# Kernel optimization log

Hardware: AMD Instinct MI355X
Metric: run time of the kernel (lower is better)

Reference implementation:

```python
import jax, jax.numpy as jnp
import numpy as np

MARGIN = 0.7
ITERS = 1000  # as hard-coded in ot_loss's log_optimal_transport call


def setup_inputs() -> dict:
    key = jax.random.key(0)
    k1, k2 = jax.random.split(key)
    # features: N x C x W x H  (query at index 0, 8 targets)
    x = jax.random.normal(k1, (9, 256, 32, 32), dtype=jnp.float32)
    # attention: N x W x H, strictly positive since it is logged directly
    att = jax.random.uniform(k2, (9, 32, 32), dtype=jnp.float32, minval=0.1, maxval=1.0)
    return {"x": x, "att": att, "label": 1}


def _ot_distance(x, att):
    N, C, W, H = x.shape
    m = W * H              # number of query locations
    n = (N - 1) * W * H    # number of target locations
    Q = x[0].reshape(C, m).T                                          # (m, C)
    T = x[1:].reshape(N - 1, C, m).transpose(0, 2, 1).reshape(n, C)   # (n, C)
    mu = att[0].reshape(m)      # query marginal
    nu = att[1:].reshape(n)     # target marginal
    # pairwise squared euclidean distances (m, n)
    M = (jnp.sum(Q * Q, axis=1)[:, None]
         + jnp.sum(T * T, axis=1)[None, :]
         - 2.0 * (Q @ T.T))
    log_mu = jnp.log(mu)
    log_nu = jnp.log(nu)

    def step(carry, _):
        u, v = carry
        u = log_mu - jax.nn.logsumexp(M + v[None, :], axis=1)
        v = log_nu - jax.nn.logsumexp(M + u[:, None], axis=0)
        return (u, v), None

    init = (jnp.zeros((m,), M.dtype), jnp.zeros((n,), M.dtype))
    (u, v), _ = jax.lax.scan(jax.checkpoint(step), init, None, length=ITERS)
    P = jnp.exp(M + u[:, None] + v[None, :])   # transport plan (m, n)
    # OT barycentric distance per query location, summed
    diff = mu[:, None] * Q - P @ T             # (m, C)
    return jnp.sqrt(jnp.sum(diff * diff, axis=1)).sum()


def reference(x, att, label):
    d = _ot_distance(x, att)
    if label:  # label is a concrete python int: positive pair
        return d
    return jnp.clip(MARGIN - d, 0.0, None)
```

## Files before the change

### kernel.cpp

```cpp
#include <hip/hip_runtime.h>
#include <math.h>

#define MR 1024
#define NC 8192
#define NCH 256
#define OT_ITERS 1000
#define IMG_STRIDE 262144
#define PBLK 512

__device__ inline float wredMax(float v){
#pragma unroll
  for (int m = 32; m >= 1; m >>= 1) v = fmaxf(v, __shfl_xor(v, m, 64));
  return v;
}
__device__ inline float wredMin(float v){
#pragma unroll
  for (int m = 32; m >= 1; m >>= 1) v = fminf(v, __shfl_xor(v, m, 64));
  return v;
}
__device__ inline float wredSum(float v){
#pragma unroll
  for (int m = 32; m >= 1; m >>= 1) v += __shfl_xor(v, m, 64);
  return v;
}

__device__ inline unsigned fkey(float f){
  unsigned b = __float_as_uint(f);
  return (b & 0x80000000u) ? ~b : (b | 0x80000000u);
}
__device__ inline float funkey(unsigned k){
  return (k & 0x80000000u) ? __uint_as_float(k & 0x7fffffffu) : __uint_as_float(~k);
}

__global__ __launch_bounds__(256) void kPrep(const float* __restrict__ x,
                                             const float* __restrict__ att,
                                             float* __restrict__ qq, float* __restrict__ tt,
                                             float* __restrict__ logmu, float* __restrict__ lognu,
                                             float* __restrict__ u, float* __restrict__ v,
                                             float* __restrict__ acc, unsigned* __restrict__ prmI,
                                             int* __restrict__ bar){
  int idx = blockIdx.x * 256 + threadIdx.x;
  if (idx < 9216){
    int img = idx >> 10, pos = idx & 1023;
    const float* p = x + img * IMG_STRIDE + pos;
    float s = 0.f;
#pragma unroll 8
    for (int c = 0; c < NCH; ++c){ float a = p[c * 1024]; s += a * a; }
    float lg = logf(att[idx]);
    if (img == 0){ qq[idx] = s;        logmu[idx] = lg; }
    else         { tt[idx - 1024] = s; lognu[idx - 1024] = lg; }
  }
  if (idx < MR) u[idx] = 0.f;
  if (idx < NC) v[idx] = 0.f;
  if (idx < 1024) bar[idx] = 0;
  if (idx == 0){ *acc = 0.f; prmI[0] = 0xFFFFFFFFu; prmI[1] = 0u; }
}

__global__ __launch_bounds__(256) void kGemmM(const float* __restrict__ x,
                                              const float* __restrict__ qq,
                                              const float* __restrict__ tt,
                                              float* __restrict__ M,
                                              unsigned* __restrict__ prmI){
  __shared__ float As[16][68];
  __shared__ float Bs[16][68];
  __shared__ float smn[4], smx[4];
  int jb = blockIdx.x;
  int ib = blockIdx.y;
  int i0 = ib * 64;
  int j0 = jb * 64;
  int k  = j0 >> 10, p0 = j0 & 1023;
  const float* A = x + i0;
  const float* B = x + (1 + k) * IMG_STRIDE + p0;
  int tid = threadIdx.x;
  int lr = tid >> 4, lc = (tid & 15) * 4;
  int ty = tid >> 4, tx = tid & 15;
  float accv[4][4] = {};
  for (int kt = 0; kt < 16; ++kt){
    int c = kt * 16 + lr;
    float4 av = *(const float4*)(A + c * 1024 + lc);
    float4 bv = *(const float4*)(B + c * 1024 + lc);
    *(float4*)(&As[lr][lc]) = av;
    *(float4*)(&Bs[lr][lc]) = bv;
    __syncthreads();
#pragma unroll
    for (int kk = 0; kk < 16; ++kk){
      float4 a = *(const float4*)(&As[kk][ty * 4]);
      float4 b = *(const float4*)(&Bs[kk][tx * 4]);
// ... 35 lines not shown
__global__ __launch_bounds__(256) void kQuantTrans(const float* __restrict__ M,
                                                   unsigned short* __restrict__ Mq,
                                                   unsigned short* __restrict__ Mtq,
                                                   float* __restrict__ prm){
  __shared__ float tile[64][65];
  const unsigned* prmI = (const unsigned*)prm;
  float mn = funkey(prmI[0]);
  float mx = funkey(prmI[1]);
  float rng = mx - mn;
  float inv = (rng > 0.f) ? 65535.0f / rng : 0.f;
  float sc  = (rng > 0.f) ? rng / 65535.0f : 0.f;
  int i0 = blockIdx.y * 64;
  int j0 = blockIdx.x * 64;
  int t = threadIdx.x;
  int tc = t & 63, tr = t >> 6;
#pragma unroll
  for (int rr = 0; rr < 64; rr += 4)
    tile[rr + tr][tc] = M[(long)(i0 + rr + tr) * NC + j0 + tc];
  __syncthreads();
#pragma unroll
  for (int rr = 0; rr < 64; rr += 4){
    float a = tile[rr + tr][tc];
    int qa = (int)lrintf((a - mn) * inv);
    qa = qa < 0 ? 0 : (qa > 65535 ? 65535 : qa);
    Mq[(long)(i0 + rr + tr) * NC + j0 + tc] = (unsigned short)qa;
    float b = tile[tc][rr + tr];
    int qb = (int)lrintf((b - mn) * inv);
    qb = qb < 0 ? 0 : (qb > 65535 ? 65535 : qb);
    Mtq[(long)(j0 + rr + tr) * MR + i0 + tc] = (unsigned short)qb;
  }
  if (blockIdx.x == 0 && blockIdx.y == 0 && t == 0){ prm[2] = mn; prm[3] = sc; }
}

__device__ inline void gbar(int* bar, int g, int ep){
  __syncthreads();
  if (threadIdx.x == 0){
    asm volatile("s_waitcnt vmcnt(0)" ::: "memory");
    int a = __hip_atomic_fetch_add(&bar[g * 32], 1, __ATOMIC_RELAXED, __HIP_MEMORY_SCOPE_AGENT);
    if (a == 64 * ep - 1){
      int go = __hip_atomic_fetch_add(&bar[512], 1, __ATOMIC_RELAXED, __HIP_MEMORY_SCOPE_AGENT);
      if (go == 8 * ep - 1){
#pragma unroll
        for (int g2 = 0; g2 < 8; ++g2)
          __hip_atomic_store(&bar[256 + g2 * 32], ep, __ATOMIC_RELAXED, __HIP_MEMORY_SCOPE_AGENT);
      }
    }
    while (__hip_atomic_load(&bar[256 + g * 32], __ATOMIC_RELAXED, __HIP_MEMORY_SCOPE_AGENT) < ep)
      __builtin_amdgcn_s_sleep(4);
  }
  __syncthreads();
}

__global__ __launch_bounds__(256, 2) void kSink2(const unsigned short* __restrict__ Mq,
                                                 const unsigned short* __restrict__ Mtq,
                                                 const float* __restrict__ logmu,
                                                 const float* __restrict__ lognu,
                                                 float* __restrict__ u,
                                                 float* __restrict__ v,
                                                 const float* __restrict__ prm,
                                                 int* __restrict__ bar){
  __shared__ float sh[8192];
  __shared__ float redA0[4], redA1[4], redB0[4], redB1[4];
  int tid = threadIdx.x, b = blockIdx.x;
  int lane = tid & 63, w = tid >> 6;
  int g = b & 7;
  float mn = prm[2], s = prm[3];
  int r0 = 2 * b;
  const unsigned short* R0 = Mq + (long)r0 * NC;
  const unsigned short* R1 = R0 + NC;
  float lmu0 = logmu[r0], lmu1 = logmu[r0 + 1];
  float lnu[4];
#pragma unroll
  for (int cc = 0; cc < 4; ++cc) lnu[cc] = lognu[16 * b + w * 4 + cc];
  int ep = 0;

  for (int it = 0; it < OT_ITERS; ++it){
#pragma unroll
    for (int h = 0; h < 2; ++h){
      float tmp[16];
#pragma unroll
      for (int q = 0; q < 16; ++q)
        tmp[q] = __hip_atomic_load(v + (h * 16 + q) * 256 + tid, __ATOMIC_RELAXED, __HIP_MEMORY_SCOPE_AGENT);
#pragma unroll
      for (int q = 0; q < 16; ++q)
        sh[(h * 16 + q) * 256 + tid] = tmp[q];
    }
    __syncthreads();
    float t0[32], t1[32];
    float mx0 = -INFINITY, mx1 = -INFINITY;
#pragma unroll
    for (int kb = 0; kb < 4; ++kb){
      int cidx = kb * 2048 + tid * 8;
      uint4 qa = *(const uint4*)(R0 + cidx);
      uint4 qb = *(const uint4*)(R1 + cidx);
      float4 v0 = *(const float4*)(&sh[cidx]);
      float4 v1 = *(const float4*)(&sh[cidx + 4]);
      float a0 = fmaf(s, (float)(qa.x & 0xFFFFu), v0.x);
      float a1 = fmaf(s, (float)(qa.x >> 16),     v0.y);
      float a2 = fmaf(s, (float)(qa.y & 0xFFFFu), v0.z);
      float a3 = fmaf(s, (float)(qa.y >> 16),     v0.w);
      float a4 = fmaf(s, (float)(qa.z & 0xFFFFu), v1.x);
      float a5 = fmaf(s, (float)(qa.z >> 16),     v1.y);
      float a6 = fmaf(s, (float)(qa.w & 0xFFFFu), v1.z);
      float a7 = fmaf(s, (float)(qa.w >> 16),     v1.w);
      float c0 = fmaf(s, (float)(qb.x & 0xFFFFu), v0.x);
      float c1 = fmaf(s, (float)(qb.x >> 16),     v0.y);
      float c2 = fmaf(s, (float)(qb.y & 0xFFFFu), v0.z);
      float c3 = fmaf(s, (float)(qb.y >> 16),     v0.w);
      float c4 = fmaf(s, (float)(qb.z & 0xFFFFu), v1.x);
      float c5 = fmaf(s, (float)(qb.z >> 16),     v1.y);
      float c6 = fmaf(s, (float)(qb.w & 0xFFFFu), v1.z);
      float c7 = fmaf(s, (float)(qb.w >> 16),     v1.w);
      t0[kb*8+0]=a0; t0[kb*8+1]=a1; t0[kb*8+2]=a2; t0[kb*8+3]=a3;
      t0[kb*8+4]=a4; t0[kb*8+5]=a5; t0[kb*8+6]=a6; t0[kb*8+7]=a7;
      t1[kb*8+0]=c0; t1[kb*8+1]=c1; t1[kb*8+2]=c2; t1[kb*8+3]=c3;
      t1[kb*8+4]=c4; t1[kb*8+5]=c5; t1[kb*8+6]=c6; t1[kb*8+7]=c7;
      mx0 = fmaxf(mx0, fmaxf(fmaxf(fmaxf(a0,a1),fmaxf(a2,a3)), fmaxf(fmaxf(a4,a5),fmaxf(a6,a7))));
      mx1 = fmaxf(mx1, fmaxf(fmaxf(fmaxf(c0,c1),fmaxf(c2,c3)), fmaxf(fmaxf(c4,c5),fmaxf(c6,c7))));
    }
    float wm0 = wredMax(mx0), wm1 = wredMax(mx1);
    if (lane == 0){ redA0[w] = wm0; redA1[w] = wm1; }
    __syncthreads();
    float bm0 = fmaxf(fmaxf(redA0[0], redA0[1]), fmaxf(redA0[2], redA0[3]));
    float bm1 = fmaxf(fmaxf(redA1[0], redA1[1]), fmaxf(redA1[2], redA1[3]));
    float s0 = 0.f, s1 = 0.f;
#pragma unroll
    for (int q = 0; q < 32; ++q){ s0 += __expf(t0[q] - bm0); s1 += __expf(t1[q] - bm1); }
    s0 = wredSum(s0); s1 = wredSum(s1);
    if (lane == 0){ redB0[w] = s0; redB1[w] = s1; }
    __syncthreads();
    if (tid == 0){
      float nu0 = lmu0 - mn - (bm0 + __logf(redB0[0] + redB0[1] + redB0[2] + redB0[3]));
      float nu1 = lmu1 - mn - (bm1 + __logf(redB1[0] + redB1[1] + redB1[2] + redB1[3]));
      __hip_atomic_store(u + r0,     nu0, __ATOMIC_RELAXED, __HIP_MEMORY_SCOPE_AGENT);
      __hip_atomic_store(u + r0 + 1, nu1, __ATOMIC_RELAXED, __HIP_MEMORY_SCOPE_AGENT);
    }
    gbar(bar, g, ++ep);

    {
      float tu[4];
#pragma unroll
      for (int q = 0; q < 4; ++q)
        tu[q] = __hip_atomic_load(u + q * 256 + tid, __ATOMIC_RELAXED, __HIP_MEMORY_SCOPE_AGENT);
#pragma unroll
      for (int q = 0; q < 4; ++q) sh[q * 256 + tid] = tu[q];
    }
    __syncthreads();
#pragma unroll
    for (int cc = 0; cc < 4; ++cc){
      int j = 16 * b + w * 4 + cc;
      const unsigned short* R = Mtq + (long)j * MR;
      uint4 qa = *(const uint4*)(R + lane * 8);
      uint4 qb = *(const uint4*)(R + 512 + lane * 8);
      float4 ua0 = *(const float4*)(&sh[lane * 8]);
      float4 ua1 = *(const float4*)(&sh[lane * 8 + 4]);
      float4 ub0 = *(const float4*)(&sh[512 + lane * 8]);
      float4 ub1 = *(const float4*)(&sh[512 + lane * 8 + 4]);
      float tv[16];
      tv[0]  = fmaf(s, (float)(qa.x & 0xFFFFu), ua0.x);
      tv[1]  = fmaf(s, (float)(qa.x >> 16),     ua0.y);
      tv[2]  = fmaf(s, (float)(qa.y & 0xFFFFu), ua0.z);
      tv[3]  = fmaf(s, (float)(qa.y >> 16),     ua0.w);
      tv[4]  = fmaf(s, (float)(qa.z & 0xFFFFu), ua1.x);
      tv[5]  = fmaf(s, (float)(qa.z >> 16),     ua1.y);
      tv[6]  = fmaf(s, (float)(qa.w & 0xFFFFu), ua1.z);
      tv[7]  = fmaf(s, (float)(qa.w >> 16),     ua1.w);
      tv[8]  = fmaf(s, (float)(qb.x & 0xFFFFu), ub0.x);
      tv[9]  = fmaf(s, (float)(qb.x >> 16),     ub0.y);
      tv[10] = fmaf(s, (float)(qb.y & 0xFFFFu), ub0.z);
      tv[11] = fmaf(s, (float)(qb.y >> 16),     ub0.w);
      tv[12] = fmaf(s, (float)(qb.z & 0xFFFFu), ub1.x);
      tv[13] = fmaf(s, (float)(qb.z >> 16),     ub1.y);
      tv[14] = fmaf(s, (float)(qb.w & 0xFFFFu), ub1.z);
      tv[15] = fmaf(s, (float)(qb.w >> 16),     ub1.w);
      float mx = -INFINITY;
#pragma unroll
      for (int q = 0; q < 16; ++q) mx = fmaxf(mx, tv[q]);
      mx = wredMax(mx);
      float sm = 0.f;
#pragma unroll
      for (int q = 0; q < 16; ++q) sm += __expf(tv[q] - mx);
      sm = wredSum(sm);
      if (lane == 0)
        __hip_atomic_store(v + j, lnu[cc] - mn - (mx + __logf(sm)),
                           __ATOMIC_RELAXED, __HIP_MEMORY_SCOPE_AGENT);
    }
    gbar(bar, g, ++ep);
  }
}

__global__ __launch_bounds__(256) void kUPassQ(const unsigned short* __restrict__ Mq,
                                               const float* __restrict__ v,
                                               const float* __restrict__ logmu,
                                               float* __restrict__ u,
                                               const float* __restrict__ prm){
  int b = blockIdx.x, tid = threadIdx.x;
  float mn = prm[2], s = prm[3];
  int r0 = 2 * b;
  const unsigned short* R0 = Mq + (long)r0 * NC;
  const unsigned short* R1 = R0 + NC;
  float t0[32], t1[32];
  float mx0 = -INFINITY, mx1 = -INFINITY;
#pragma unroll
  for (int kb = 0; kb < 4; ++kb){
    int cidx = kb * 2048 + tid * 8;
    uint4 qa = *(const uint4*)(R0 + cidx);
    uint4 qb = *(const uint4*)(R1 + cidx);
    float4 v0 = *(const float4*)(v + cidx);
    float4 v1 = *(const float4*)(v + cidx + 4);
    float a0 = fmaf(s, (float)(qa.x & 0xFFFFu), v0.x);
    float a1 = fmaf(s, (float)(qa.x >> 16),     v0.y);
    float a2 = fmaf(s, (float)(qa.y & 0xFFFFu), v0.z);
    float a3 = fmaf(s, (float)(qa.y >> 16),     v0.w);
    float a4 = fmaf(s, (float)(qa.z & 0xFFFFu), v1.x);
    float a5 = fmaf(s, (float)(qa.z >> 16),     v1.y);
    float a6 = fmaf(s, (float)(qa.w & 0xFFFFu), v1.z);
    float a7 = fmaf(s, (float)(qa.w >> 16),     v1.w);
    float c0 = fmaf(s, (float)(qb.x & 0xFFFFu), v0.x);
    float c1 = fmaf(s, (float)(qb.x >> 16),     v0.y);
    float c2 = fmaf(s, (float)(qb.y & 0xFFFFu), v0.z);
    float c3 = fmaf(s, (float)(qb.y >> 16),     v0.w);
    float c4 = fmaf(s, (float)(qb.z & 0xFFFFu), v1.x);
    float c5 = fmaf(s, (float)(qb.z >> 16),     v1.y);
    float c6 = fmaf(s, (float)(qb.w & 0xFFFFu), v1.z);
    float c7 = fmaf(s, (float)(qb.w >> 16),     v1.w);
    t0[kb*8+0]=a0; t0[kb*8+1]=a1; t0[kb*8+2]=a2; t0[kb*8+3]=a3;
    t0[kb*8+4]=a4; t0[kb*8+5]=a5; t0[kb*8+6]=a6; t0[kb*8+7]=a7;
    t1[kb*8+0]=c0; t1[kb*8+1]=c1; t1[kb*8+2]=c2; t1[kb*8+3]=c3;
    t1[kb*8+4]=c4; t1[kb*8+5]=c5; t1[kb*8+6]=c6; t1[kb*8+7]=c7;
    mx0 = fmaxf(mx0, fmaxf(fmaxf(fmaxf(a0,a1),fmaxf(a2,a3)), fmaxf(fmaxf(a4,a5),fmaxf(a6,a7))));
    mx1 = fmaxf(mx1, fmaxf(fmaxf(fmaxf(c0,c1),fmaxf(c2,c3)), fmaxf(fmaxf(c4,c5),fmaxf(c6,c7))));
  }
  __shared__ float redA0[4], redA1[4], redB0[4], redB1[4];
  int lane = tid & 63, w = tid >> 6;
  float wm0 = wredMax(mx0), wm1 = wredMax(mx1);
  if (lane == 0){ redA0[w] = wm0; redA1[w] = wm1; }
  __syncthreads();
  float bm0 = fmaxf(fmaxf(redA0[0], redA0[1]), fmaxf(redA0[2], redA0[3]));
  float bm1 = fmaxf(fmaxf(redA1[0], redA1[1]), fmaxf(redA1[2], redA1[3]));
  float s0 = 0.f, s1 = 0.f;
#pragma unroll
  for (int q = 0; q < 32; ++q){ s0 += __expf(t0[q] - bm0); s1 += __expf(t1[q] - bm1); }
  s0 = wredSum(s0); s1 = wredSum(s1);
  if (lane == 0){ redB0[w] = s0; redB1[w] = s1; }
  __syncthreads();
  if (tid == 0){
    u[r0]     = logmu[r0]     - mn - (bm0 + __logf(redB0[0] + redB0[1] + redB0[2] + redB0[3]));
    u[r0 + 1] = logmu[r0 + 1] - mn - (bm1 + __logf(redB1[0] + redB1[1] + redB1[2] + redB1[3]));
  }
}

__global__ __launch_bounds__(256) void kVPassQ(const unsigned short* __restrict__ Mtq,
                                               const float* __restrict__ u,
                                               const float* __restrict__ lognu,
                                               float* __restrict__ v,
                                               const float* __restrict__ prm){
  __shared__ float ulds[1024];
  int tid = threadIdx.x;
  float mn = prm[2], s = prm[3];
  *(float4*)(&ulds[tid * 4]) = *(const float4*)(u + tid * 4);
  __syncthreads();
  int w = tid >> 6, lane = tid & 63;
#pragma unroll
  for (int cc = 0; cc < 4; ++cc){
    int j = blockIdx.x * 16 + w * 4 + cc;
    const unsigned short* R = Mtq + (long)j * MR;
    uint4 qa = *(const uint4*)(R + lane * 8);
    uint4 qb = *(const uint4*)(R + 512 + lane * 8);
    float4 ua0 = *(const float4*)(&ulds[lane * 8]);
    float4 ua1 = *(const float4*)(&ulds[lane * 8 + 4]);
    float4 ub0 = *(const float4*)(&ulds[512 + lane * 8]);
    float4 ub1 = *(const float4*)(&ulds[512 + lane * 8 + 4]);
    float tv[16];
    tv[0]  = fmaf(s, (float)(qa.x & 0xFFFFu), ua0.x);
    tv[1]  = fmaf(s, (float)(qa.x >> 16),     ua0.y);
    tv[2]  = fmaf(s, (float)(qa.y & 0xFFFFu), ua0.z);
    tv[3]  = fmaf(s, (float)(qa.y >> 16),     ua0.w);
    tv[4]  = fmaf(s, (float)(qa.z & 0xFFFFu), ua1.x);
    tv[5]  = fmaf(s, (float)(qa.z >> 16),     ua1.y);
    tv[6]  = fmaf(s, (float)(qa.w & 0xFFFFu), ua1.z);
    tv[7]  = fmaf(s, (float)(qa.w >> 16),     ua1.w);
    tv[8]  = fmaf(s, (float)(qb.x & 0xFFFFu), ub0.x);
    tv[9]  = fmaf(s, (float)(qb.x >> 16),     ub0.y);
    tv[10] = fmaf(s, (float)(qb.y & 0xFFFFu), ub0.z);
    tv[11] = fmaf(s, (float)(qb.y >> 16),     ub0.w);
    tv[12] = fmaf(s, (float)(qb.z & 0xFFFFu), ub1.x);
    tv[13] = fmaf(s, (float)(qb.z >> 16),     ub1.y);
    tv[14] = fmaf(s, (float)(qb.w & 0xFFFFu), ub1.z);
    tv[15] = fmaf(s, (float)(qb.w >> 16),     ub1.w);
    float mx = -INFINITY;
#pragma unroll
    for (int q = 0; q < 16; ++q) mx = fmaxf(mx, tv[q]);
    mx = wredMax(mx);
    float sm = 0.f;
#pragma unroll
    for (int q = 0; q < 16; ++q) sm += __expf(tv[q] - mx);
    sm = wredSum(sm);
    if (lane == 0) v[j] = lognu[j] - mn - (mx + __logf(sm));
  }
}

__global__ __launch_bounds__(256) void kFinal(const float* __restrict__ x,
                                              const float* __restrict__ att,
                                              const float* __restrict__ M,
                                              const float* __restrict__ u,
                                              const float* __restrict__ v,
                                              float* __restrict__ acc){
  __shared__ float pch[4][256];
  __shared__ float redS[4];
  int tid = threadIdx.x;
  int r0 = blockIdx.x * 4;
  float u4[4];
#pragma unroll
  for (int rr = 0; rr < 4; ++rr) u4[rr] = u[r0 + rr];
  float o[4] = {0.f, 0.f, 0.f, 0.f};
  for (int jc = 0; jc < NC; jc += 256){
    float vv = v[jc + tid];
#pragma unroll
    for (int rr = 0; rr < 4; ++rr)
      pch[rr][tid] = __expf(M[(long)(r0 + rr) * NC + jc + tid] + u4[rr] + vv);
    __syncthreads();
    int k = jc >> 10;
    const float* Tp = x + (1 + k) * IMG_STRIDE + tid * 1024 + (jc & 1023);
    for (int jj = 0; jj < 256; jj += 4){
      float4 tv = *(const float4*)(Tp + jj);
      float tq[4] = {tv.x, tv.y, tv.z, tv.w};
#pragma unroll
      for (int q = 0; q < 4; ++q){
        o[0] += pch[0][jj + q] * tq[q];
        o[1] += pch[1][jj + q] * tq[q];
        o[2] += pch[2][jj + q] * tq[q];
        o[3] += pch[3][jj + q] * tq[q];
      }
    }
    __syncthreads();
  }
  int lane = tid & 63, wid = tid >> 6;
  float dtot = 0.f;
#pragma unroll
  for (int rr = 0; rr < 4; ++rr){
    float mu = att[r0 + rr];
    float qv = x[tid * 1024 + (r0 + rr)];
    float diff = mu * qv - o[rr];
    float wsum = wredSum(diff * diff);
    if (lane == 0) redS[wid] = wsum;
    __syncthreads();
    if (tid == 0) dtot += sqrtf(redS[0] + redS[1] + redS[2] + redS[3]);
    __syncthreads();
  }
  if (tid == 0) atomicAdd(acc, dtot);
}

__global__ void kOut(const float* __restrict__ acc, const int* __restrict__ label,
                     float* __restrict__ out){
  if (threadIdx.x == 0 && blockIdx.x == 0){
    float d = *acc;
    out[0] = (*label) ? d : fmaxf(0.7f - d, 0.f);
  }
}

extern "C" void kernel_launch(void* const* d_in, const int* in_sizes, int n_in,
                              void* d_out, int out_size, void* d_ws, size_t ws_size,
                              hipStream_t stream){
  const float* x   = (const float*)d_in[0];
  const float* att = (const float*)d_in[1];
  const int* label = (const int*)d_in[2];
  float* W = (float*)d_ws;
  float* out = (float*)d_out;

  float* M = W;
  unsigned short* Mq  = (unsigned short*)(W + 8388608);
  unsigned short* Mtq = (unsigned short*)(W + 8388608 + 4194304);
  float* S     = W + 16777216;
  float* qq    = S;
  float* tt    = qq + 1024;
  float* logmu = tt + 8192;
  float* lognu = logmu + 1024;
  float* u     = lognu + 8192;
  float* v     = u + 1024;
  float* acc   = v + 8192;
  float* prm   = acc + 1;
  unsigned* prmI = (unsigned*)prm;
  int*   bar   = (int*)(prm + 4);

  hipLaunchKernelGGL(kPrep, dim3(37), dim3(256), 0, stream, x, att, qq, tt, logmu, lognu, u, v, acc, prmI, bar);
  hipLaunchKernelGGL(kGemmM, dim3(128, 16), dim3(256), 0, stream, x, qq, tt, M, prmI);
  hipLaunchKernelGGL(kQuantTrans, dim3(128, 16), dim3(256), 0, stream, M, Mq, Mtq, prm);

  void* args[] = { (void*)&Mq, (void*)&Mtq, (void*)&logmu, (void*)&lognu,
                   (void*)&u, (void*)&v, (void*)&prm, (void*)&bar };
  hipError_t rc = hipLaunchCooperativeKernel((const void*)kSink2,
                                             dim3(PBLK), dim3(256), args, 0, stream);
  if (rc != hipSuccess){
    for (int it = 0; it < OT_ITERS; ++it){
      hipLaunchKernelGGL(kUPassQ, dim3(512), dim3(256), 0, stream, Mq, v, logmu, u, prm);
      hipLaunchKernelGGL(kVPassQ, dim3(512), dim3(256), 0, stream, Mtq, u, lognu, v, prm);
    }
  }
  hipLaunchKernelGGL(kFinal, dim3(256), dim3(256), 0, stream, x, att, M, u, v, acc);
  hipLaunchKernelGGL(kOut, dim3(1), dim3(1), 0, stream, acc, label, out);
}
```

Before: 11.86 ms.

## Widen persistent Sinkhorn blocks to 512 threads and drop LDS staging

The cooperative Sinkhorn kernel now runs 512 threads per block. Each thread handles 16 contiguous columns, and each wave handles two v-rows instead of four. The shared-memory staging of u and v and its __syncthreads are removed, and each thread loads its slice directly with 64-bit atomic loads. This aims to cut per-iteration latency between grid barriers through more parallelism and fewer block syncs, at the cost of higher register pressure from the 512-thread launch bounds and redundant global reads of u across waves.

```diff
diff --git a/kernel.cpp b/kernel.cpp
--- a/kernel.cpp
+++ b/kernel.cpp
@@ -30,6 +30,15 @@
 }
 __device__ inline float funkey(unsigned k){
   return (k & 0x80000000u) ? __uint_as_float(k & 0x7fffffffu) : __uint_as_float(~k);
+}
+
+__device__ inline float2 aload2(const float* p){
+  unsigned long long q = __hip_atomic_load((const unsigned long long*)p,
+                                           __ATOMIC_RELAXED, __HIP_MEMORY_SCOPE_AGENT);
+  float2 r;
+  r.x = __uint_as_float((unsigned)(q & 0xFFFFFFFFull));
+  r.y = __uint_as_float((unsigned)(q >> 32));
+  return r;
 }
 
 __global__ __launch_bounds__(256) void kPrep(const float* __restrict__ x,
@@ -173,7 +182,21 @@
   __syncthreads();
 }
 
-__global__ __launch_bounds__(256, 2) void kSink2(const unsigned short* __restrict__ Mq,
+#define DQ8(d, base, q4, o) \
+  d[(base)+0] = fmaf(s, (float)((q4).x & 0xFFFFu), o[(base)+0]); \
+  d[(base)+1] = fmaf(s, (float)((q4).x >> 16),     o[(base)+1]); \
+  d[(base)+2] = fmaf(s, (float)((q4).y & 0xFFFFu), o[(base)+2]); \
+  d[(base)+3] = fmaf(s, (float)((q4).y >> 16),     o[(base)+3]); \
+  d[(base)+4] = fmaf(s, (float)((q4).z & 0xFFFFu), o[(base)+4]); \
+  d[(base)+5] = fmaf(s, (float)((q4).z >> 16),     o[(base)+5]); \
+  d[(base)+6] = fmaf(s, (float)((q4).w & 0xFFFFu), o[(base)+6]); \
+  d[(base)+7] = fmaf(s, (float)((q4).w >> 16),     o[(base)+7]);
+
+#define MAX16(a) \
+  fmaxf(fmaxf(fmaxf(fmaxf(a[0],a[1]),fmaxf(a[2],a[3])),fmaxf(fmaxf(a[4],a[5]),fmaxf(a[6],a[7]))), \
+        fmaxf(fmaxf(fmaxf(a[8],a[9]),fmaxf(a[10],a[11])),fmaxf(fmaxf(a[12],a[13]),fmaxf(a[14],a[15]))))
+
+__global__ __launch_bounds__(512, 4) void kSink2(const unsigned short* __restrict__ Mq,
                                                  const unsigned short* __restrict__ Mtq,
                                                  const float* __restrict__ logmu,
                                                  const float* __restrict__ lognu,
@@ -181,130 +204,98 @@
                                                  float* __restrict__ v,
                                                  const float* __restrict__ prm,
                                                  int* __restrict__ bar){
-  __shared__ float sh[8192];
-  __shared__ float redA0[4], redA1[4], redB0[4], redB1[4];
+  __shared__ float redA0[8], redA1[8], redB0[8], redB1[8];
   int tid = threadIdx.x, b = blockIdx.x;
   int lane = tid & 63, w = tid >> 6;
   int g = b & 7;
   float mn = prm[2], s = prm[3];
   int r0 = 2 * b;
-  const unsigned short* R0 = Mq + (long)r0 * NC;
+  const unsigned short* R0 = Mq + (long)r0 * NC + tid * 16;
   const unsigned short* R1 = R0 + NC;
   float lmu0 = logmu[r0], lmu1 = logmu[r0 + 1];
-  float lnu[4];
-#pragma unroll
-  for (int cc = 0; cc < 4; ++cc) lnu[cc] = lognu[16 * b + w * 4 + cc];
+  int jA = 16 * b + 2 * w, jB = jA + 1;
+  float lnuA = lognu[jA], lnuB = lognu[jB];
+  const unsigned short* RA = Mtq + (long)jA * MR + lane * 16;
+  const unsigned short* RB = RA + MR;
+  const float* vp = v + tid * 16;
+  const float* up = u + lane * 16;
   int ep = 0;
 
   for (int it = 0; it < OT_ITERS; ++it){
-#pragma unroll
-    for (int h = 0; h < 2; ++h){
-      float tmp[16];
-#pragma unroll
-      for (int q = 0; q < 16; ++q)
-        tmp[q] = __hip_atomic_load(v + (h * 16 + q) * 256 + tid, __ATOMIC_RELAXED, __HIP_MEMORY_SCOPE_AGENT);
-#pragma unroll
-      for (int q = 0; q < 16; ++q)
-        sh[(h * 16 + q) * 256 + tid] = tmp[q];
-    }
-    __syncthreads();
-    float t0[32], t1[32];
-    float mx0 = -INFINITY, mx1 = -INFINITY;
-#pragma unroll
-    for (int kb = 0; kb < 4; ++kb){
-      int cidx = kb * 2048 + tid * 8;
-      uint4 qa = *(const uint4*)(R0 + cidx);
-      uint4 qb = *(const uint4*)(R1 + cidx);
-      float4 v0 = *(const float4*)(&sh[cidx]);
-      float4 v1 = *(const float4*)(&sh[cidx + 4]);
-      float a0 = fmaf(s, (float)(qa.x & 0xFFFFu), v0.x);
-      float a1 = fmaf(s, (float)(qa.x >> 16),     v0.y);
-      float a2 = fmaf(s, (float)(qa.y & 0xFFFFu), v0.z);
-      float a3 = fmaf(s, (float)(qa.y >> 16),     v0.w);
-      float a4 = fmaf(s, (float)(qa.z & 0xFFFFu), v1.x);
-      float a5 = fmaf(s, (float)(qa.z >> 16),     v1.y);
-      float a6 = fmaf(s, (float)(qa.w & 0xFFFFu), v1.z);
-      float a7 = fmaf(s, (float)(qa.w >> 16),     v1.w);
-      float c0 = fmaf(s, (float)(qb.x & 0xFFFFu), v0.x);
-      float c1 = fmaf(s, (float)(qb.x >> 16),     v0.y);
-      float c2 = fmaf(s, (float)(qb.y & 0xFFFFu), v0.z);
-      float c3 = fmaf(s, (float)(qb.y >> 16),     v0.w);
-      float c4 = fmaf(s, (float)(qb.z & 0xFFFFu), v1.x);
-      float c5 = fmaf(s, (float)(qb.z >> 16),     v1.y);
-      float c6 = fmaf(s, (float)(qb.w & 0xFFFFu), v1.z);
-      float c7 = fmaf(s, (float)(qb.w >> 16),     v1.w);
-      t0[kb*8+0]=a0; t0[kb*8+1]=a1; t0[kb*8+2]=a2; t0[kb*8+3]=a3;
-      t0[kb*8+4]=a4; t0[kb*8+5]=a5; t0[kb*8+6]=a6; t0[kb*8+7]=a7;
-      t1[kb*8+0]=c0; t1[kb*8+1]=c1; t1[kb*8+2]=c2; t1[kb*8+3]=c3;
-      t1[kb*8+4]=c4; t1[kb*8+5]=c5; t1[kb*8+6]=c6; t1[kb*8+7]=c7;
-      mx0 = fmaxf(mx0, fmaxf(fmaxf(fmaxf(a0,a1),fmaxf(a2,a3)), fmaxf(fmaxf(a4,a5),fmaxf(a6,a7))));
-      mx1 = fmaxf(mx1, fmaxf(fmaxf(fmaxf(c0,c1),fmaxf(c2,c3)), fmaxf(fmaxf(c4,c5),fmaxf(c6,c7))));
-    }
+    float va[16];
+#pragma unroll
+    for (int q = 0; q < 8; ++q){
+      float2 p = aload2(vp + 2 * q);
+      va[2 * q] = p.x; va[2 * q + 1] = p.y;
+    }
+    uint4 qa0 = *(const uint4*)(R0);
+    uint4 qa1 = *(const uint4*)(R0 + 8);
+    uint4 qb0 = *(const uint4*)(R1);
+    uint4 qb1 = *(const uint4*)(R1 + 8);
+    float t0[16], t1[16];
+    DQ8(t0, 0, qa0, va); DQ8(t0, 8, qa1, va);
+    DQ8(t1, 0, qb0, va); DQ8(t1, 8, qb1, va);
+    float mx0 = MAX16(t0);
+    float mx1 = MAX16(t1);
     float wm0 = wredMax(mx0), wm1 = wredMax(mx1);
     if (lane == 0){ redA0[w] = wm0; redA1[w] = wm1; }
     __syncthreads();
-    float bm0 = fmaxf(fmaxf(redA0[0], redA0[1]), fmaxf(redA0[2], redA0[3]));
-    float bm1 = fmaxf(fmaxf(redA1[0], redA1[1]), fmaxf(redA1[2], redA1[3]));
+    float bm0 = fmaxf(fmaxf(fmaxf(redA0[0], redA0[1]), fmaxf(redA0[2], redA0[3])),
+                      fmaxf(fmaxf(redA0[4], redA0[5]), fmaxf(redA0[6], redA0[7])));
+    float bm1 = fmaxf(fmaxf(fmaxf(redA1[0], redA1[1]), fmaxf(redA1[2], redA1[3])),
+                      fmaxf(fmaxf(redA1[4], redA1[5]), fmaxf(redA1[6], redA1[7])));
     float s0 = 0.f, s1 = 0.f;
 #pragma unroll
-    for (int q = 0; q < 32; ++q){ s0 += __expf(t0[q] - bm0); s1 += __expf(t1[q] - bm1); }
+    for (int q = 0; q < 16; ++q){ s0 += __expf(t0[q] - bm0); s1 += __expf(t1[q] - bm1); }
     s0 = wredSum(s0); s1 = wredSum(s1);
     if (lane == 0){ redB0[w] = s0; redB1[w] = s1; }
     __syncthreads();
     if (tid == 0){
-      float nu0 = lmu0 - mn - (bm0 + __logf(redB0[0] + redB0[1] + redB0[2] + redB0[3]));
-      float nu1 = lmu1 - mn - (bm1 + __logf(redB1[0] + redB1[1] + redB1[2] + redB1[3]));
+      float sb0 = (redB0[0] + redB0[1]) + (redB0[2] + redB0[3])
+                + (redB0[4] + redB0[5]) + (redB0[6] + redB0[7]);
+      float sb1 = (redB1[0] + redB1[1]) + (redB1[2] + redB1[3])
+                + (redB1[4] + redB1[5]) + (redB1[6] + redB1[7]);
+      float nu0 = lmu0 - mn - (bm0 + __logf(sb0));
+      float nu1 = lmu1 - mn - (bm1 + __logf(sb1));
       __hip_atomic_store(u + r0,     nu0, __ATOMIC_RELAXED, __HIP_MEMORY_SCOPE_AGENT);
       __hip_atomic_store(u + r0 + 1, nu1, __ATOMIC_RELAXED, __HIP_MEMORY_SCOPE_AGENT);
     }
     gbar(bar, g, ++ep);
 
+    float ua[16];
+#pragma unroll
+    for (int q = 0; q < 8; ++q){
+      float2 p = aload2(up + 2 * q);
+      ua[2 * q] = p.x; ua[2 * q + 1] = p.y;
+    }
     {
-      float tu[4];
-#pragma unroll
-      for (int q = 0; q < 4; ++q)
-        tu[q] = __hip_atomic_load(u + q * 256 + tid, __ATOMIC_RELAXED, __HIP_MEMORY_SCOPE_AGENT);
-#pragma unroll
-      for (int q = 0; q < 4; ++q) sh[q * 256 + tid] = tu[q];
-    }
-    __syncthreads();
-#pragma unroll
-    for (int cc = 0; cc < 4; ++cc){
-      int j = 16 * b + w * 4 + cc;
-      const unsigned short* R = Mtq + (long)j * MR;
-      uint4 qa = *(const uint4*)(R + lane * 8);
-      uint4 qb = *(const uint4*)(R + 512 + lane * 8);
-      float4 ua0 = *(const float4*)(&sh[lane * 8]);
-      float4 ua1 = *(const float4*)(&sh[lane * 8 + 4]);
-      float4 ub0 = *(const float4*)(&sh[512 + lane * 8]);
-      float4 ub1 = *(const float4*)(&sh[512 + lane * 8 + 4]);
+      uint4 ca0 = *(const uint4*)(RA);
+      uint4 ca1 = *(const uint4*)(RA + 8);
       float tv[16];
-      tv[0]  = fmaf(s, (float)(qa.x & 0xFFFFu), ua0.x);
-      tv[1]  = fmaf(s, (float)(qa.x >> 16),     ua0.y);
-      tv[2]  = fmaf(s, (float)(qa.y & 0xFFFFu), ua0.z);
-      tv[3]  = fmaf(s, (float)(qa.y >> 16),     ua0.w);
-      tv[4]  = fmaf(s, (float)(qa.z & 0xFFFFu), ua1.x);
-      tv[5]  = fmaf(s, (float)(qa.z >> 16),     ua1.y);
-      tv[6]  = fmaf(s, (float)(qa.w & 0xFFFFu), ua1.z);
-      tv[7]  = fmaf(s, (float)(qa.w >> 16),     ua1.w);
-      tv[8]  = fmaf(s, (float)(qb.x & 0xFFFFu), ub0.x);
-      tv[9]  = fmaf(s, (float)(qb.x >> 16),     ub0.y);
-      tv[10] = fmaf(s, (float)(qb.y & 0xFFFFu), ub0.z);
-      tv[11] = fmaf(s, (float)(qb.y >> 16),     ub0.w);
-      tv[12] = fmaf(s, (float)(qb.z & 0xFFFFu), ub1.x);
-      tv[13] = fmaf(s, (float)(qb.z >> 16),     ub1.y);
-      tv[14] = fmaf(s, (float)(qb.w & 0xFFFFu), ub1.z);
-      tv[15] = fmaf(s, (float)(qb.w >> 16),     ub1.w);
-      float mx = -INFINITY;
-#pragma unroll
-      for (int q = 0; q < 16; ++q) mx = fmaxf(mx, tv[q]);
+      DQ8(tv, 0, ca0, ua); DQ8(tv, 8, ca1, ua);
+      float mx = MAX16(tv);
       mx = wredMax(mx);
       float sm = 0.f;
 #pragma unroll
       for (int q = 0; q < 16; ++q) sm += __expf(tv[q] - mx);
       sm = wredSum(sm);
       if (lane == 0)
-        __hip_atomic_store(v + j, lnu[cc] - mn - (mx + __logf(sm)),
+        __hip_atomic_store(v + jA, lnuA - mn - (mx + __logf(sm)),
+                           __ATOMIC_RELAXED, __HIP_MEMORY_SCOPE_AGENT);
+    }
+    {
+      uint4 cb0 = *(const uint4*)(RB);
+      uint4 cb1 = *(const uint4*)(RB + 8);
+      float tv[16];
+      DQ8(tv, 0, cb0, ua); DQ8(tv, 8, cb1, ua);
+      float mx = MAX16(tv);
+      mx = wredMax(mx);
+      float sm = 0.f;
+#pragma unroll
+      for (int q = 0; q < 16; ++q) sm += __expf(tv[q] - mx);
+      sm = wredSum(sm);
+      if (lane == 0)
+        __hip_atomic_store(v + jB, lnuB - mn - (mx + __logf(sm)),
                            __ATOMIC_RELAXED, __HIP_MEMORY_SCOPE_AGENT);
     }
     gbar(bar, g, ++ep);
@@ -512,7 +503,7 @@
   void* args[] = { (void*)&Mq, (void*)&Mtq, (void*)&logmu, (void*)&lognu,
                    (void*)&u, (void*)&v, (void*)&prm, (void*)&bar };
   hipError_t rc = hipLaunchCooperativeKernel((const void*)kSink2,
-                                             dim3(PBLK), dim3(256), args, 0, stream);
+                                             dim3(PBLK), dim3(512), args, 0, stream);
   if (rc != hipSuccess){
     for (int it = 0; it < OT_ITERS; ++it){
       hipLaunchKernelGGL(kUPassQ, dim3(512), dim3(256), 0, stream, Mq, v, logmu, u, prm);
```

Result: slower. 15.92 ms (+34.3%).

## Replace grid barriers with epoch-tagged u/v values for dataflow synchronization

Applied to the files above, without the earlier changes.

Removes the two hierarchical atomic grid barriers per Sinkhorn iteration in the cooperative kernel. Each u and v value is now stored as a 64-bit word holding the float and an iteration epoch. Consumers spin until every value they read carries the current epoch, so blocks wait only on the data they need instead of on all blocks. This doubles the bytes of u/v traffic and adds per-element polling. There is also a possible hazard that v entries get overwritten for iteration it+1 while slower blocks are still reading iteration it values.

```diff
diff --git a/kernel.cpp b/kernel.cpp
--- a/kernel.cpp
+++ b/kernel.cpp
@@ -32,13 +32,24 @@
   return (k & 0x80000000u) ? __uint_as_float(k & 0x7fffffffu) : __uint_as_float(~k);
 }
 
+__device__ inline unsigned long long aload64(const unsigned long long* p){
+  return __hip_atomic_load(p, __ATOMIC_RELAXED, __HIP_MEMORY_SCOPE_AGENT);
+}
+__device__ inline void astore64(unsigned long long* p, unsigned long long x){
+  __hip_atomic_store(p, x, __ATOMIC_RELAXED, __HIP_MEMORY_SCOPE_AGENT);
+}
+__device__ inline unsigned long long packVE(float val, int ep){
+  return (unsigned long long)__float_as_uint(val) |
+         ((unsigned long long)(unsigned)ep << 32);
+}
+
 __global__ __launch_bounds__(256) void kPrep(const float* __restrict__ x,
                                              const float* __restrict__ att,
                                              float* __restrict__ qq, float* __restrict__ tt,
                                              float* __restrict__ logmu, float* __restrict__ lognu,
-                                             float* __restrict__ u, float* __restrict__ v,
-                                             float* __restrict__ acc, unsigned* __restrict__ prmI,
-                                             int* __restrict__ bar){
+                                             unsigned long long* __restrict__ u2t,
+                                             unsigned long long* __restrict__ v2t,
+                                             float* __restrict__ acc, unsigned* __restrict__ prmI){
   int idx = blockIdx.x * 256 + threadIdx.x;
   if (idx < 9216){
     int img = idx >> 10, pos = idx & 1023;
@@ -50,9 +61,8 @@
     if (img == 0){ qq[idx] = s;        logmu[idx] = lg; }
     else         { tt[idx - 1024] = s; lognu[idx - 1024] = lg; }
   }
-  if (idx < MR) u[idx] = 0.f;
-  if (idx < NC) v[idx] = 0.f;
-  if (idx < 1024) bar[idx] = 0;
+  if (idx < MR) u2t[idx] = 0ull;
+  if (idx < NC) v2t[idx] = 0ull;
   if (idx == 0){ *acc = 0.f; prmI[0] = 0xFFFFFFFFu; prmI[1] = 0u; }
 }
 
@@ -154,38 +164,27 @@
   if (blockIdx.x == 0 && blockIdx.y == 0 && t == 0){ prm[2] = mn; prm[3] = sc; }
 }
 
-__device__ inline void gbar(int* bar, int g, int ep){
-  __syncthreads();
-  if (threadIdx.x == 0){
-    asm volatile("s_waitcnt vmcnt(0)" ::: "memory");
-    int a = __hip_atomic_fetch_add(&bar[g * 32], 1, __ATOMIC_RELAXED, __HIP_MEMORY_SCOPE_AGENT);
-    if (a == 64 * ep - 1){
-      int go = __hip_atomic_fetch_add(&bar[512], 1, __ATOMIC_RELAXED, __HIP_MEMORY_SCOPE_AGENT);
-      if (go == 8 * ep - 1){
-#pragma unroll
-        for (int g2 = 0; g2 < 8; ++g2)
-          __hip_atomic_store(&bar[256 + g2 * 32], ep, __ATOMIC_RELAXED, __HIP_MEMORY_SCOPE_AGENT);
-      }
-    }
-    while (__hip_atomic_load(&bar[256 + g * 32], __ATOMIC_RELAXED, __HIP_MEMORY_SCOPE_AGENT) < ep)
-      __builtin_amdgcn_s_sleep(4);
-  }
-  __syncthreads();
-}
-
-__global__ __launch_bounds__(256, 2) void kSink2(const unsigned short* __restrict__ Mq,
+#define DQV8(t, base, q4, v0, v1) \
+  t[(base)+0] = fmaf(s, (float)((q4).x & 0xFFFFu), (v0).x); \
+  t[(base)+1] = fmaf(s, (float)((q4).x >> 16),     (v0).y); \
+  t[(base)+2] = fmaf(s, (float)((q4).y & 0xFFFFu), (v0).z); \
+  t[(base)+3] = fmaf(s, (float)((q4).y >> 16),     (v0).w); \
+  t[(base)+4] = fmaf(s, (float)((q4).z & 0xFFFFu), (v1).x); \
+  t[(base)+5] = fmaf(s, (float)((q4).z >> 16),     (v1).y); \
+  t[(base)+6] = fmaf(s, (float)((q4).w & 0xFFFFu), (v1).z); \
+  t[(base)+7] = fmaf(s, (float)((q4).w >> 16),     (v1).w);
+
+__global__ __launch_bounds__(256, 2) void kSink4(const unsigned short* __restrict__ Mq,
                                                  const unsigned short* __restrict__ Mtq,
                                                  const float* __restrict__ logmu,
                                                  const float* __restrict__ lognu,
-                                                 float* __restrict__ u,
-                                                 float* __restrict__ v,
-                                                 const float* __restrict__ prm,
-                                                 int* __restrict__ bar){
+                                                 unsigned long long* __restrict__ u2t,
+                                                 unsigned long long* __restrict__ v2t,
+                                                 const float* __restrict__ prm){
   __shared__ float sh[8192];
   __shared__ float redA0[4], redA1[4], redB0[4], redB1[4];
   int tid = threadIdx.x, b = blockIdx.x;
   int lane = tid & 63, w = tid >> 6;
-  int g = b & 7;
   float mn = prm[2], s = prm[3];
   int r0 = 2 * b;
   const unsigned short* R0 = Mq + (long)r0 * NC;
@@ -194,20 +193,31 @@
   float lnu[4];
 #pragma unroll
   for (int cc = 0; cc < 4; ++cc) lnu[cc] = lognu[16 * b + w * 4 + cc];
-  int ep = 0;
 
   for (int it = 0; it < OT_ITERS; ++it){
 #pragma unroll
     for (int h = 0; h < 2; ++h){
-      float tmp[16];
+      unsigned long long P[16];
 #pragma unroll
       for (int q = 0; q < 16; ++q)
-        tmp[q] = __hip_atomic_load(v + (h * 16 + q) * 256 + tid, __ATOMIC_RELAXED, __HIP_MEMORY_SCOPE_AGENT);
+        P[q] = aload64(v2t + (h * 16 + q) * 256 + tid);
+      for (;;){
+        int bad = 0;
+#pragma unroll
+        for (int q = 0; q < 16; ++q)
+          if ((unsigned)(P[q] >> 32) < (unsigned)it){
+            bad = 1;
+            P[q] = aload64(v2t + (h * 16 + q) * 256 + tid);
+          }
+        if (!bad) break;
+        __builtin_amdgcn_s_sleep(1);
+      }
 #pragma unroll
       for (int q = 0; q < 16; ++q)
-        sh[(h * 16 + q) * 256 + tid] = tmp[q];
-    }
-    __syncthreads();
+        sh[(h * 16 + q) * 256 + tid] = __uint_as_float((unsigned)P[q]);
+    }
+    __syncthreads();
+
     float t0[32], t1[32];
     float mx0 = -INFINITY, mx1 = -INFINITY;
 #pragma unroll
@@ -217,28 +227,13 @@
       uint4 qb = *(const uint4*)(R1 + cidx);
       float4 v0 = *(const float4*)(&sh[cidx]);
       float4 v1 = *(const float4*)(&sh[cidx + 4]);
-      float a0 = fmaf(s, (float)(qa.x & 0xFFFFu), v0.x);
-      float a1 = fmaf(s, (float)(qa.x >> 16),     v0.y);
-      float a2 = fmaf(s, (float)(qa.y & 0xFFFFu), v0.z);
-      float a3 = fmaf(s, (float)(qa.y >> 16),     v0.w);
-      float a4 = fmaf(s, (float)(qa.z & 0xFFFFu), v1.x);
-      float a5 = fmaf(s, (float)(qa.z >> 16),     v1.y);
-      float a6 = fmaf(s, (float)(qa.w & 0xFFFFu), v1.z);
-      float a7 = fmaf(s, (float)(qa.w >> 16),     v1.w);
-      float c0 = fmaf(s, (float)(qb.x & 0xFFFFu), v0.x);
-      float c1 = fmaf(s, (float)(qb.x >> 16),     v0.y);
-      float c2 = fmaf(s, (float)(qb.y & 0xFFFFu), v0.z);
-      float c3 = fmaf(s, (float)(qb.y >> 16),     v0.w);
-      float c4 = fmaf(s, (float)(qb.z & 0xFFFFu), v1.x);
-      float c5 = fmaf(s, (float)(qb.z >> 16),     v1.y);
-      float c6 = fmaf(s, (float)(qb.w & 0xFFFFu), v1.z);
-      float c7 = fmaf(s, (float)(qb.w >> 16),     v1.w);
-      t0[kb*8+0]=a0; t0[kb*8+1]=a1; t0[kb*8+2]=a2; t0[kb*8+3]=a3;
-      t0[kb*8+4]=a4; t0[kb*8+5]=a5; t0[kb*8+6]=a6; t0[kb*8+7]=a7;
-      t1[kb*8+0]=c0; t1[kb*8+1]=c1; t1[kb*8+2]=c2; t1[kb*8+3]=c3;
-      t1[kb*8+4]=c4; t1[kb*8+5]=c5; t1[kb*8+6]=c6; t1[kb*8+7]=c7;
-      mx0 = fmaxf(mx0, fmaxf(fmaxf(fmaxf(a0,a1),fmaxf(a2,a3)), fmaxf(fmaxf(a4,a5),fmaxf(a6,a7))));
-      mx1 = fmaxf(mx1, fmaxf(fmaxf(fmaxf(c0,c1),fmaxf(c2,c3)), fmaxf(fmaxf(c4,c5),fmaxf(c6,c7))));
+      DQV8(t0, kb * 8, qa, v0, v1);
+      DQV8(t1, kb * 8, qb, v0, v1);
+#pragma unroll
+      for (int q = 0; q < 8; ++q){
+        mx0 = fmaxf(mx0, t0[kb * 8 + q]);
+        mx1 = fmaxf(mx1, t1[kb * 8 + q]);
+      }
     }
     float wm0 = wredMax(mx0), wm1 = wredMax(mx1);
     if (lane == 0){ redA0[w] = wm0; redA1[w] = wm1; }
@@ -254,20 +249,32 @@
     if (tid == 0){
       float nu0 = lmu0 - mn - (bm0 + __logf(redB0[0] + redB0[1] + redB0[2] + redB0[3]));
       float nu1 = lmu1 - mn - (bm1 + __logf(redB1[0] + redB1[1] + redB1[2] + redB1[3]));
-      __hip_atomic_store(u + r0,     nu0, __ATOMIC_RELAXED, __HIP_MEMORY_SCOPE_AGENT);
-      __hip_atomic_store(u + r0 + 1, nu1, __ATOMIC_RELAXED, __HIP_MEMORY_SCOPE_AGENT);
-    }
-    gbar(bar, g, ++ep);
+      astore64(u2t + r0,     packVE(nu0, it + 1));
+      astore64(u2t + r0 + 1, packVE(nu1, it + 1));
+    }
 
     {
-      float tu[4];
+      unsigned long long PU[4];
 #pragma unroll
       for (int q = 0; q < 4; ++q)
-        tu[q] = __hip_atomic_load(u + q * 256 + tid, __ATOMIC_RELAXED, __HIP_MEMORY_SCOPE_AGENT);
-#pragma unroll
-      for (int q = 0; q < 4; ++q) sh[q * 256 + tid] = tu[q];
-    }
-    __syncthreads();
+        PU[q] = aload64(u2t + q * 256 + tid);
+      for (;;){
+        int bad = 0;
+#pragma unroll
+        for (int q = 0; q < 4; ++q)
+          if ((unsigned)(PU[q] >> 32) < (unsigned)(it + 1)){
+            bad = 1;
+            PU[q] = aload64(u2t + q * 256 + tid);
+          }
+        if (!bad) break;
+        __builtin_amdgcn_s_sleep(1);
+      }
+#pragma unroll
+      for (int q = 0; q < 4; ++q)
+        sh[q * 256 + tid] = __uint_as_float((unsigned)PU[q]);
+    }
+    __syncthreads();
+
 #pragma unroll
     for (int cc = 0; cc < 4; ++cc){
       int j = 16 * b + w * 4 + cc;
@@ -279,22 +286,8 @@
       float4 ub0 = *(const float4*)(&sh[512 + lane * 8]);
       float4 ub1 = *(const float4*)(&sh[512 + lane * 8 + 4]);
       float tv[16];
-      tv[0]  = fmaf(s, (float)(qa.x & 0xFFFFu), ua0.x);
-      tv[1]  = fmaf(s, (float)(qa.x >> 16),     ua0.y);
-      tv[2]  = fmaf(s, (float)(qa.y & 0xFFFFu), ua0.z);
-      tv[3]  = fmaf(s, (float)(qa.y >> 16),     ua0.w);
-      tv[4]  = fmaf(s, (float)(qa.z & 0xFFFFu), ua1.x);
-      tv[5]  = fmaf(s, (float)(qa.z >> 16),     ua1.y);
-      tv[6]  = fmaf(s, (float)(qa.w & 0xFFFFu), ua1.z);
-      tv[7]  = fmaf(s, (float)(qa.w >> 16),     ua1.w);
-      tv[8]  = fmaf(s, (float)(qb.x & 0xFFFFu), ub0.x);
-      tv[9]  = fmaf(s, (float)(qb.x >> 16),     ub0.y);
-      tv[10] = fmaf(s, (float)(qb.y & 0xFFFFu), ub0.z);
-      tv[11] = fmaf(s, (float)(qb.y >> 16),     ub0.w);
-      tv[12] = fmaf(s, (float)(qb.z & 0xFFFFu), ub1.x);
-      tv[13] = fmaf(s, (float)(qb.z >> 16),     ub1.y);
-      tv[14] = fmaf(s, (float)(qb.w & 0xFFFFu), ub1.z);
-      tv[15] = fmaf(s, (float)(qb.w >> 16),     ub1.w);
+      DQV8(tv, 0, qa, ua0, ua1);
+      DQV8(tv, 8, qb, ub0, ub1);
       float mx = -INFINITY;
 #pragma unroll
       for (int q = 0; q < 16; ++q) mx = fmaxf(mx, tv[q]);
@@ -304,23 +297,23 @@
       for (int q = 0; q < 16; ++q) sm += __expf(tv[q] - mx);
       sm = wredSum(sm);
       if (lane == 0)
-        __hip_atomic_store(v + j, lnu[cc] - mn - (mx + __logf(sm)),
-                           __ATOMIC_RELAXED, __HIP_MEMORY_SCOPE_AGENT);
-    }
-    gbar(bar, g, ++ep);
+        astore64(v2t + j, packVE(lnu[cc] - mn - (mx + __logf(sm)), it + 1));
+    }
+    __syncthreads();
   }
 }
 
 __global__ __launch_bounds__(256) void kUPassQ(const unsigned short* __restrict__ Mq,
-                                               const float* __restrict__ v,
+                                               const unsigned long long* __restrict__ v2t,
                                                const float* __restrict__ logmu,
-                                               float* __restrict__ u,
+                                               unsigned long long* __restrict__ u2t,
                                                const float* __restrict__ prm){
   int b = blockIdx.x, tid = threadIdx.x;
   float mn = prm[2], s = prm[3];
   int r0 = 2 * b;
   const unsigned short* R0 = Mq + (long)r0 * NC;
   const unsigned short* R1 = R0 + NC;
+  const uint2* V2 = (const uint2*)v2t;
   float t0[32], t1[32];
   float mx0 = -INFINITY, mx1 = -INFINITY;
 #pragma unroll
@@ -328,30 +321,21 @@
     int cidx = kb * 2048 + tid * 8;
     uint4 qa = *(const uint4*)(R0 + cidx);
     uint4 qb = *(const uint4*)(R1 + cidx);
-    float4 v0 = *(const float4*)(v + cidx);
-    float4 v1 = *(const float4*)(v + cidx + 4);
-    float a0 = fmaf(s, (float)(qa.x & 0xFFFFu), v0.x);
-    float a1 = fmaf(s, (float)(qa.x >> 16),     v0.y);
-    float a2 = fmaf(s, (float)(qa.y & 0xFFFFu), v0.z);
-    float a3 = fmaf(s, (float)(qa.y >> 16),     v0.w);
-    float a4 = fmaf(s, (float)(qa.z & 0xFFFFu), v1.x);
-    float a5 = fmaf(s, (float)(qa.z >> 16),     v1.y);
-    float a6 = fmaf(s, (float)(qa.w & 0xFFFFu), v1.z);
-    float a7 = fmaf(s, (float)(qa.w >> 16),     v1.w);
-    float c0 = fmaf(s, (float)(qb.x & 0xFFFFu), v0.x);
-    float c1 = fmaf(s, (float)(qb.x >> 16),     v0.y);
-    float c2 = fmaf(s, (float)(qb.y & 0xFFFFu), v0.z);
-    float c3 = fmaf(s, (float)(qb.y >> 16),     v0.w);
-    float c4 = fmaf(s, (float)(qb.z & 0xFFFFu), v1.x);
-    float c5 = fmaf(s, (float)(qb.z >> 16),     v1.y);
-    float c6 = fmaf(s, (float)(qb.w & 0xFFFFu), v1.z);
-    float c7 = fmaf(s, (float)(qb.w >> 16),     v1.w);
-    t0[kb*8+0]=a0; t0[kb*8+1]=a1; t0[kb*8+2]=a2; t0[kb*8+3]=a3;
-    t0[kb*8+4]=a4; t0[kb*8+5]=a5; t0[kb*8+6]=a6; t0[kb*8+7]=a7;
-    t1[kb*8+0]=c0; t1[kb*8+1]=c1; t1[kb*8+2]=c2; t1[kb*8+3]=c3;
-    t1[kb*8+4]=c4; t1[kb*8+5]=c5; t1[kb*8+6]=c6; t1[kb*8+7]=c7;
-    mx0 = fmaxf(mx0, fmaxf(fmaxf(fmaxf(a0,a1),fmaxf(a2,a3)), fmaxf(fmaxf(a4,a5),fmaxf(a6,a7))));
-    mx1 = fmaxf(mx1, fmaxf(fmaxf(fmaxf(c0,c1),fmaxf(c2,c3)), fmaxf(fmaxf(c4,c5),fmaxf(c6,c7))));
+    uint4 p0 = *(const uint4*)(V2 + cidx);
+    uint4 p1 = *(const uint4*)(V2 + cidx + 2);
+    uint4 p2 = *(const uint4*)(V2 + cidx + 4);
+    uint4 p3 = *(const uint4*)(V2 + cidx + 6);
+    float4 v0 = { __uint_as_float(p0.x), __uint_as_float(p0.z),
+                  __uint_as_float(p1.x), __uint_as_float(p1.z) };
+    float4 v1 = { __uint_as_float(p2.x), __uint_as_float(p2.z),
+                  __uint_as_float(p3.x), __uint_as_float(p3.z) };
+    DQV8(t0, kb * 8, qa, v0, v1);
+    DQV8(t1, kb * 8, qb, v0, v1);
+#pragma unroll
+    for (int q = 0; q < 8; ++q){
+      mx0 = fmaxf(mx0, t0[kb * 8 + q]);
+      mx1 = fmaxf(mx1, t1[kb * 8 + q]);
+    }
   }
   __shared__ float redA0[4], redA1[4], redB0[4], redB1[4];
   int lane = tid & 63, w = tid >> 6;
@@ -367,20 +351,26 @@
   if (lane == 0){ redB0[w] = s0; redB1[w] = s1; }
   __syncthreads();
   if (tid == 0){
-    u[r0]     = logmu[r0]     - mn - (bm0 + __logf(redB0[0] + redB0[1] + redB0[2] + redB0[3]));
-    u[r0 + 1] = logmu[r0 + 1] - mn - (bm1 + __logf(redB1[0] + redB1[1] + redB1[2] + redB1[3]));
+    u2t[r0]     = packVE(logmu[r0]     - mn - (bm0 + __logf(redB0[0]+redB0[1]+redB0[2]+redB0[3])), 1);
+    u2t[r0 + 1] = packVE(logmu[r0 + 1] - mn - (bm1 + __logf(redB1[0]+redB1[1]+redB1[2]+redB1[3])), 1);
   }
 }
 
 __global__ __launch_bounds__(256) void kVPassQ(const unsigned short* __restrict__ Mtq,
-                                               const float* __restrict__ u,
+                                               const unsigned long long* __restrict__ u2t,
                                                const float* __restrict__ lognu,
-                                               float* __restrict__ v,
+                                               unsigned long long* __restrict__ v2t,
                                                const float* __restrict__ prm){
   __shared__ float ulds[1024];
   int tid = threadIdx.x;
   float mn = prm[2], s = prm[3];
-  *(float4*)(&ulds[tid * 4]) = *(const float4*)(u + tid * 4);
+  const uint2* U2 = (const uint2*)u2t;
+  uint4 pu0 = *(const uint4*)(U2 + tid * 4);
+  uint4 pu1 = *(const uint4*)(U2 + tid * 4 + 2);
+  ulds[tid * 4 + 0] = __uint_as_float(pu0.x);
+  ulds[tid * 4 + 1] = __uint_as_float(pu0.z);
+  ulds[tid * 4 + 2] = __uint_as_float(pu1.x);
+  ulds[tid * 4 + 3] = __uint_as_float(pu1.z);
   __syncthreads();
   int w = tid >> 6, lane = tid & 63;
 #pragma unroll
@@ -394,22 +384,8 @@
     float4 ub0 = *(const float4*)(&ulds[512 + lane * 8]);
     float4 ub1 = *(const float4*)(&ulds[512 + lane * 8 + 4]);
     float tv[16];
-    tv[0]  = fmaf(s, (float)(qa.x & 0xFFFFu), ua0.x);
-    tv[1]  = fmaf(s, (float)(qa.x >> 16),     ua0.y);
-    tv[2]  = fmaf(s, (float)(qa.y & 0xFFFFu), ua0.z);
-    tv[3]  = fmaf(s, (float)(qa.y >> 16),     ua0.w);
-    tv[4]  = fmaf(s, (float)(qa.z & 0xFFFFu), ua1.x);
-    tv[5]  = fmaf(s, (float)(qa.z >> 16),     ua1.y);
-    tv[6]  = fmaf(s, (float)(qa.w & 0xFFFFu), ua1.z);
-    tv[7]  = fmaf(s, (float)(qa.w >> 16),     ua1.w);
-    tv[8]  = fmaf(s, (float)(qb.x & 0xFFFFu), ub0.x);
-    tv[9]  = fmaf(s, (float)(qb.x >> 16),     ub0.y);
-    tv[10] = fmaf(s, (float)(qb.y & 0xFFFFu), ub0.z);
-    tv[11] = fmaf(s, (float)(qb.y >> 16),     ub0.w);
-    tv[12] = fmaf(s, (float)(qb.z & 0xFFFFu), ub1.x);
-    tv[13] = fmaf(s, (float)(qb.z >> 16),     ub1.y);
-    tv[14] = fmaf(s, (float)(qb.w & 0xFFFFu), ub1.z);
-    tv[15] = fmaf(s, (float)(qb.w >> 16),     ub1.w);
+    DQV8(tv, 0, qa, ua0, ua1);
+    DQV8(tv, 8, qb, ub0, ub1);
     float mx = -INFINITY;
 #pragma unroll
     for (int q = 0; q < 16; ++q) mx = fmaxf(mx, tv[q]);
@@ -418,26 +394,28 @@
 #pragma unroll
     for (int q = 0; q < 16; ++q) sm += __expf(tv[q] - mx);
     sm = wredSum(sm);
-    if (lane == 0) v[j] = lognu[j] - mn - (mx + __logf(sm));
+    if (lane == 0) v2t[j] = packVE(lognu[j] - mn - (mx + __logf(sm)), 1);
   }
 }
 
 __global__ __launch_bounds__(256) void kFinal(const float* __restrict__ x,
                                               const float* __restrict__ att,
                                               const float* __restrict__ M,
-                                              const float* __restrict__ u,
-                                              const float* __restrict__ v,
+                                              const unsigned long long* __restrict__ u2t,
+                                              const unsigned long long* __restrict__ v2t,
                                               float* __restrict__ acc){
   __shared__ float pch[4][256];
   __shared__ float redS[4];
   int tid = threadIdx.x;
   int r0 = blockIdx.x * 4;
+  const uint2* U2 = (const uint2*)u2t;
+  const uint2* V2 = (const uint2*)v2t;
   float u4[4];
 #pragma unroll
-  for (int rr = 0; rr < 4; ++rr) u4[rr] = u[r0 + rr];
+  for (int rr = 0; rr < 4; ++rr) u4[rr] = __uint_as_float(U2[r0 + rr].x);
   float o[4] = {0.f, 0.f, 0.f, 0.f};
   for (int jc = 0; jc < NC; jc += 256){
-    float vv = v[jc + tid];
+    float vv = __uint_as_float(V2[jc + tid].x);
 #pragma unroll
     for (int rr = 0; rr < 4; ++rr)
       pch[rr][tid] = __expf(M[(long)(r0 + rr) * NC + jc + tid] + u4[rr] + vv);
@@ -493,32 +471,31 @@
   float* M = W;
   unsigned short* Mq  = (unsigned short*)(W + 8388608);
   unsigned short* Mtq = (unsigned short*)(W + 8388608 + 4194304);
-  float* S     = W + 16777216;
+  unsigned long long* u2t = (unsigned long long*)(W + 16777216);
+  unsigned long long* v2t = u2t + MR;
+  float* S     = W + 16777216 + 2 * (MR + NC);
   float* qq    = S;
   float* tt    = qq + 1024;
   float* logmu = tt + 8192;
   float* lognu = logmu + 1024;
-  float* u     = lognu + 8192;
-  float* v     = u + 1024;
-  float* acc   = v + 8192;
+  float* acc   = lognu + 8192;
   float* prm   = acc + 1;
   unsigned* prmI = (unsigned*)prm;
-  int*   bar   = (int*)(prm + 4);
-
-  hipLaunchKernelGGL(kPrep, dim3(37), dim3(256), 0, stream, x, att, qq, tt, logmu, lognu, u, v, acc, prmI, bar);
+
+  hipLaunchKernelGGL(kPrep, dim3(37), dim3(256), 0, stream, x, att, qq, tt, logmu, lognu, u2t, v2t, acc, prmI);
   hipLaunchKernelGGL(kGemmM, dim3(128, 16), dim3(256), 0, stream, x, qq, tt, M, prmI);
   hipLaunchKernelGGL(kQuantTrans, dim3(128, 16), dim3(256), 0, stream, M, Mq, Mtq, prm);
 
   void* args[] = { (void*)&Mq, (void*)&Mtq, (void*)&logmu, (void*)&lognu,
-                   (void*)&u, (void*)&v, (void*)&prm, (void*)&bar };
-  hipError_t rc = hipLaunchCooperativeKernel((const void*)kSink2,
+                   (void*)&u2t, (void*)&v2t, (void*)&prm };
+  hipError_t rc = hipLaunchCooperativeKernel((const void*)kSink4,
                                              dim3(PBLK), dim3(256), args, 0, stream);
   if (rc != hipSuccess){
     for (int it = 0; it < OT_ITERS; ++it){
-      hipLaunchKernelGGL(kUPassQ, dim3(512), dim3(256), 0, stream, Mq, v, logmu, u, prm);
-      hipLaunchKernelGGL(kVPassQ, dim3(512), dim3(256), 0, stream, Mtq, u, lognu, v, prm);
-    }
-  }
-  hipLaunchKernelGGL(kFinal, dim3(256), dim3(256), 0, stream, x, att, M, u, v, acc);
+      hipLaunchKernelGGL(kUPassQ, dim3(512), dim3(256), 0, stream, Mq, v2t, logmu, u2t, prm);
+      hipLaunchKernelGGL(kVPassQ, dim3(512), dim3(256), 0, stream, Mtq, u2t, lognu, v2t, prm);
+    }
+  }
+  hipLaunchKernelGGL(kFinal, dim3(256), dim3(256), 0, stream, x, att, M, u2t, v2t, acc);
   hipLaunchKernelGGL(kOut, dim3(1), dim3(1), 0, stream, acc, label, out);
 }
```

After: 18.94 ms. 1.6x slower.
